# Optimization experiments

Measured on AMD Instinct MI355X. Metric: run time of the kernel, lower is better.

Reference implementation:

```python
import jax, jax.numpy as jnp
import numpy as np

N = 8192
F_IN = 256
F_OUT = 64
ALPHA = 0.2  # LeakyReLU negative slope
MASK_VAL = -9e15


def setup_inputs() -> dict:
    key = jax.random.key(0)
    k1, k2, k3, k4 = jax.random.split(key, 4)
    h = jax.random.normal(k1, (N, F_IN), dtype=jnp.float32)
    adj = jax.random.randint(k2, (N, N), 0, 2, dtype=jnp.int32)  # 0/1 dense adjacency
    # Parameters (original creates them inside forward with xavier init; here fixed inputs)
    W = jax.random.normal(k3, (F_IN, F_OUT), dtype=jnp.float32) * (1.414 * np.sqrt(2.0 / (F_IN + F_OUT)))
    a = jax.random.normal(k4, (2 * F_OUT, 1), dtype=jnp.float32) * (1.414 * np.sqrt(2.0 / (2 * F_OUT + 1)))
    return {"h": h, "adj": adj, "W": W, "a": a}


def reference(h, adj, W, a):
    # Wh: [N, F_OUT]
    Wh = h @ W
    # e_ij = LeakyReLU(a^T [Wh_i ; Wh_j]) computed via broadcast instead of the
    f_src = Wh @ a[:F_OUT, 0]   # [N] contribution of row node i
    f_dst = Wh @ a[F_OUT:, 0]   # [N] contribution of col node j
    e = jax.nn.leaky_relu(f_src[:, None] + f_dst[None, :], negative_slope=ALPHA)  # [N, N]
    # adj-masked row softmax
    scores = jnp.where(adj > 0, e, MASK_VAL)
    attention = jax.nn.softmax(scores, axis=1)
    # dropout omitted (deterministic eval reference)
    h_prime = attention @ Wh  # [N, F_OUT]
    return jax.nn.elu(h_prime)  # concat=True branch
```

## Files before the change

kernel.cpp:

```cpp
#include <hip/hip_runtime.h>
#include <hip/hip_bf16.h>

#define NN 8192
#define FIN 256
#define FOUT 64
#define L2E 1.4426950408889634f
#define PADK3 136

typedef __attribute__((ext_vector_type(8))) short short8;
typedef __attribute__((ext_vector_type(4))) float f32x4;
typedef __attribute__((ext_vector_type(4))) int   iv4;

#define BAR() do { \
  __asm__ __volatile__("s_waitcnt lgkmcnt(0)" ::: "memory"); \
  __builtin_amdgcn_s_barrier(); \
  __asm__ __volatile__("" ::: "memory"); \
} while (0)

__device__ __forceinline__ unsigned short f2bf(float x){
  unsigned u = __float_as_uint(x);
  u += 0x7FFFu + ((u >> 16) & 1u);
  return (unsigned short)(u >> 16);
}

__device__ __forceinline__ unsigned spread4(unsigned x){
  x &= 0xFFu;
  x = (x | (x << 12)) & 0x000F000Fu;
  x = (x | (x << 6))  & 0x03030303u;
  x = (x | (x << 3))  & 0x11111111u;
  return x;
}

__device__ __forceinline__ void cv_process(iv4 d, int l,
                                           unsigned* __restrict__ mp, int g){
  unsigned n = (unsigned)(d.x != 0)        | ((unsigned)(d.y != 0) << 1)
             | ((unsigned)(d.z != 0) << 2) | ((unsigned)(d.w != 0) << 3);
  unsigned long long B0 = __ballot((n & 1u) != 0);
  unsigned long long B1 = __ballot((n & 2u) != 0);
  unsigned long long B2 = __ballot((n & 4u) != 0);
  unsigned long long B3 = __ballot((n & 8u) != 0);
  const int hi = l & 4, sh = (l & 3) * 8;
  unsigned b0 = (unsigned)((hi ? (B0 >> 32) : B0) >> sh);
  unsigned b1 = (unsigned)((hi ? (B1 >> 32) : B1) >> sh);
  unsigned b2 = (unsigned)((hi ? (B2 >> 32) : B2) >> sh);
  unsigned b3 = (unsigned)((hi ? (B3 >> 32) : B3) >> sh);
  unsigned word = spread4(b0) | (spread4(b1) << 1)
                | (spread4(b2) << 2) | (spread4(b3) << 3);
  if (l < 8) mp[g*8 + l] = word;
}

__global__ __launch_bounds__(256) void k_pm(const float* __restrict__ h,
    const float* __restrict__ W, const float* __restrict__ a,
    const int* __restrict__ adj, unsigned short* __restrict__ WhT,
    float* __restrict__ fs, float* __restrict__ fd,
    unsigned* __restrict__ gmax_u, unsigned* __restrict__ mask){
  const int bid = blockIdx.x, t = threadIdx.x;
  const int l = t & 63, wv = t >> 6;
  if (bid % 3 == 0){
    const int pid = bid / 3;
    __shared__ float Ws[128*64];
    __shared__ float hs[8][128];
    const int rb = pid * 8;
    float acc0 = 0.f, acc1 = 0.f;
    for (int half = 0; half < 2; ++half){
      if (half) __syncthreads();
      for (int i = t; i < 2048; i += 256)
        ((float4*)Ws)[i] = ((const float4*)W)[half*2048 + i];
      {
        int rr = t >> 5, cc = t & 31;
        ((float4*)&hs[rr][0])[cc] =
            *(const float4*)(h + (size_t)(rb+rr)*FIN + half*128 + cc*4);
      }
      __syncthreads();
      #pragma unroll 8
      for (int k = 0; k < 128; ++k){
        float wval = Ws[k*64 + l];
        acc0 = fmaf(hs[wv*2+0][k], wval, acc0);
        acc1 = fmaf(hs[wv*2+1][k], wval, acc1);
      }
    }
    const int r0 = rb + wv*2, r1 = r0 + 1;
    float a1 = a[l], a2 = a[64 + l];
    float p0 = acc0*a1, q0 = acc0*a2, p1 = acc1*a1, q1 = acc1*a2;
    #pragma unroll
    for (int m = 1; m < 64; m <<= 1){
      p0 += __shfl_xor(p0, m); q0 += __shfl_xor(q0, m);
      p1 += __shfl_xor(p1, m); q1 += __shfl_xor(q1, m);
    }
    if (l == 0){
      fs[r0] = p0*L2E; fs[r1] = p1*L2E; fd[r0] = q0*L2E; fd[r1] = q1*L2E;
      atomicMax(gmax_u, __float_as_uint(q0*L2E + 64.0f));
      atomicMax(gmax_u, __float_as_uint(q1*L2E + 64.0f));
    }
    WhT[(size_t)l*NN + r0] = f2bf(acc0);
    WhT[(size_t)l*NN + r1] = f2bf(acc1);
  } else {
    const int cid = bid - bid/3 - 1;
    const unsigned rowid = (unsigned)cid*4u + (unsigned)wv;
    const iv4* __restrict__ ap = (const iv4*)(adj + (size_t)rowid*8192u) + l;
    unsigned* __restrict__ mp = mask + rowid*256u;
    iv4 d0 = ap[0*64], d1 = ap[1*64], d2 = ap[2*64], d3 = ap[3*64];
    iv4 d4 = ap[4*64], d5 = ap[5*64], d6 = ap[6*64], d7 = ap[7*64];
    #pragma unroll 1
    for (int i = 0; i < 32; i += 8){
      cv_process(d0, l, mp, i+0); if (i+ 8 < 32) d0 = ap[(i+ 8)*64];
      cv_process(d1, l, mp, i+1); if (i+ 9 < 32) d1 = ap[(i+ 9)*64];
      cv_process(d2, l, mp, i+2); if (i+10 < 32) d2 = ap[(i+10)*64];
      cv_process(d3, l, mp, i+3); if (i+11 < 32) d3 = ap[(i+11)*64];
      cv_process(d4, l, mp, i+4); if (i+12 < 32) d4 = ap[(i+12)*64];
      cv_process(d5, l, mp, i+5); if (i+13 < 32) d5 = ap[(i+13)*64];
      cv_process(d6, l, mp, i+6); if (i+14 < 32) d6 = ap[(i+14)*64];
      cv_process(d7, l, mp, i+7); if (i+15 < 32) d7 = ap[(i+15)*64];
    }
  }
}

__device__ __forceinline__ void attn_math(unsigned mbits, f32x4 fv0, f32x4 fv1,
    short8 w0, short8 w1, short8 w2, short8 w3,
    float fsrL, float mL, f32x4* acc, float& s0, float& s1){
  const float fv[8] = {fv0[0],fv0[1],fv0[2],fv0[3], fv1[0],fv1[1],fv1[2],fv1[3]};
  float w[8];
  #pragma unroll
  for (int j = 0; j < 8; ++j){
    float x  = fsrL + fv[j];
    float tt = fmaxf(x, 0.2f*x);
    float e  = __builtin_amdgcn_exp2f(tt - mL);
    w[j] = (mbits & (1u << j)) ? e : 0.0f;
  }
  s0 += (w[0]+w[2]) + (w[4]+w[6]);
  s1 += (w[1]+w[3]) + (w[5]+w[7]);
  short8 af;
  __hip_bfloat162* afp = (__hip_bfloat162*)&af;
  #pragma unroll
  for (int j = 0; j < 4; ++j)
    afp[j] = __float22bfloat162_rn(make_float2(w[2*j], w[2*j+1]));
  acc[0] = __builtin_amdgcn_mfma_f32_16x16x32_bf16(af, w0, acc[0], 0,0,0);
  acc[1] = __builtin_amdgcn_mfma_f32_16x16x32_bf16(af, w1, acc[1], 0,0,0);
  acc[2] = __builtin_amdgcn_mfma_f32_16x16x32_bf16(af, w2, acc[2], 0,0,0);
  acc[3] = __builtin_amdgcn_mfma_f32_16x16x32_bf16(af, w3, acc[3], 0,0,0);
}

__device__ __forceinline__ void attn_sub(const unsigned short* __restrict__ bs,
    const float* __restrict__ fsl, int sub, int row, int qsh, unsigned mword,
    float fsrL, float mL, f32x4* acc, float& s0, float& s1){
  const int o = sub*32 + qsh;
  f32x4 fv0 = *(const f32x4*)&fsl[o];
  f32x4 fv1 = *(const f32x4*)&fsl[o + 4];
  short8 w0 = *(const short8*)&bs[( 0 + row)*PADK3 + o];
  short8 w1 = *(const short8*)&bs[(16 + row)*PADK3 + o];
  short8 w2 = *(const short8*)&bs[(32 + row)*PADK3 + o];
  short8 w3 = *(const short8*)&bs[(48 + row)*PADK3 + o];
  attn_math(mword >> qsh, fv0, fv1, w0, w1, w2, w3, fsrL, mL, acc, s0, s1);
}

__global__ __launch_bounds__(256, 4) void k_attn(const unsigned* __restrict__ mask,
    const unsigned short* __restrict__ WhT, const float* __restrict__ fs,
    const float* __restrict__ fd, const unsigned* __restrict__ gmax_u,
    float* __restrict__ acc_out, float* __restrict__ s_out){
  __shared__ unsigned short bslab[2][64*PADK3];
  __shared__ float fslab[2][128];
  const int t = threadIdx.x, l = t & 63, wv = t >> 6;
  const int g = blockIdx.x & 127;
  const int kchunk = blockIdx.x >> 7;
  const int row = l & 15, quad = l >> 4;
  const int ibase = g*64 + wv*16;
  const int irow  = ibase + row;
  const float gmaxL = __uint_as_float(*gmax_u) - 64.0f;
  const float fsrL  = fs[irow];
  const float xL    = fsrL + gmaxL;
  const float mL    = fmaxf(xL, 0.2f*xL);

  const unsigned jbase = (unsigned)kchunk*1024u;
  const uint4* __restrict__ mq =
      (const uint4*)(mask + (size_t)irow*256u + (jbase >> 5));
  const unsigned sg_off = (unsigned)l*8192u + jbase + (unsigned)wv*32u;
  const int      sl_off = l*PADK3 + wv*32;
  const int      qsh    = quad*8;

  f32x4 acc[4];
  #pragma unroll
  for (int nb = 0; nb < 4; ++nb) acc[nb] = (f32x4){0.f,0.f,0.f,0.f};

  {
    const unsigned short* p = WhT + sg_off;
    *(short8*)&bslab[0][sl_off]      = *(const short8*)(p);
    *(short8*)&bslab[0][sl_off + 8]  = *(const short8*)(p + 8);
    *(short8*)&bslab[0][sl_off + 16] = *(const short8*)(p + 16);
    *(short8*)&bslab[0][sl_off + 24] = *(const short8*)(p + 24);
    if (t < 128) fslab[0][t] = fd[jbase + t];
  }
  uint4 M0 = mq[0];
  uint4 M1 = mq[1];

  float s0 = 0.f, s1 = 0.f;
  short8 nw0, nw1, nw2, nw3; float nf = 0.f;

  #pragma unroll 1
  for (int s = 0; s < 8; s += 2){
    BAR();
    {
      const unsigned short* p = WhT + sg_off + (s+1)*128;
      nw0 = *(const short8*)(p);
      nw1 = *(const short8*)(p + 8);
      nw2 = *(const short8*)(p + 16);
      nw3 = *(const short8*)(p + 24);
    }
    if (t < 128) nf = fd[jbase + (s+1)*128 + t];
    attn_sub(bslab[0], fslab[0], 0, row, qsh, M0.x, fsrL, mL, acc, s0, s1);
    attn_sub(bslab[0], fslab[0], 1, row, qsh, M0.y, fsrL, mL, acc, s0, s1);
    attn_sub(bslab[0], fslab[0], 2, row, qsh, M0.z, fsrL, mL, acc, s0, s1);
    attn_sub(bslab[0], fslab[0], 3, row, qsh, M0.w, fsrL, mL, acc, s0, s1);
    if (s + 2 < 8) M0 = mq[s + 2];
    *(short8*)&bslab[1][sl_off]      = nw0;
    *(short8*)&bslab[1][sl_off + 8]  = nw1;
    *(short8*)&bslab[1][sl_off + 16] = nw2;
    *(short8*)&bslab[1][sl_off + 24] = nw3;
    if (t < 128) fslab[1][t] = nf;

    BAR();
    if (s + 2 < 8){
      const unsigned short* p = WhT + sg_off + (s+2)*128;
      nw0 = *(const short8*)(p);
      nw1 = *(const short8*)(p + 8);
      nw2 = *(const short8*)(p + 16);
      nw3 = *(const short8*)(p + 24);
      nf = (t < 128) ? fd[jbase + (s+2)*128 + t] : 0.f;
    }
    attn_sub(bslab[1], fslab[1], 0, row, qsh, M1.x, fsrL, mL, acc, s0, s1);
    attn_sub(bslab[1], fslab[1], 1, row, qsh, M1.y, fsrL, mL, acc, s0, s1);
    attn_sub(bslab[1], fslab[1], 2, row, qsh, M1.z, fsrL, mL, acc, s0, s1);
    attn_sub(bslab[1], fslab[1], 3, row, qsh, M1.w, fsrL, mL, acc, s0, s1);
    if (s + 3 < 8) M1 = mq[s + 3];
    if (s + 2 < 8){
      *(short8*)&bslab[0][sl_off]      = nw0;
      *(short8*)&bslab[0][sl_off + 8]  = nw1;
      *(short8*)&bslab[0][sl_off + 16] = nw2;
      *(short8*)&bslab[0][sl_off + 24] = nw3;
      if (t < 128) fslab[0][t] = nf;
    }
  }

  float sacc = s0 + s1;
  sacc += __shfl_xor(sacc, 16);
  sacc += __shfl_xor(sacc, 32);
  if (l < 16) s_out[kchunk*NN + ibase + l] = sacc;
  float* op = acc_out + ((size_t)kchunk*NN + ibase)*FOUT;
  #pragma unroll
  for (int nb = 0; nb < 4; ++nb)
    #pragma unroll
    for (int r = 0; r < 4; ++r)
      op[(quad*4 + r)*FOUT + nb*16 + row] = acc[nb][r];
}

__global__ __launch_bounds__(256) void k_out(const float* __restrict__ acc,
    const float* __restrict__ s, float* __restrict__ out){
  const int idx4 = blockIdx.x*256 + threadIdx.x;
  const int i = idx4 >> 4;
  float4 num = make_float4(0.f,0.f,0.f,0.f);
  float den = 0.f;
  #pragma unroll
  for (int ks = 0; ks < 8; ++ks){
    float4 v = ((const float4*)acc)[idx4 + ks*(NN*FOUT/4)];
    num.x += v.x; num.y += v.y; num.z += v.z; num.w += v.w;
    den += s[i + ks*NN];
  }
  const float rd = 1.0f / den;
  float4 o;
  float x;
  x = num.x*rd; o.x = (x > 0.f) ? x : (__expf(x) - 1.0f);
  x = num.y*rd; o.y = (x > 0.f) ? x : (__expf(x) - 1.0f);
  x = num.z*rd; o.z = (x > 0.f) ? x : (__expf(x) - 1.0f);
  x = num.w*rd; o.w = (x > 0.f) ? x : (__expf(x) - 1.0f);
  ((float4*)out)[idx4] = o;
}

extern "C" void kernel_launch(void* const* d_in, const int* in_sizes, int n_in,
                              void* d_out, int out_size, void* d_ws, size_t ws_size,
                              hipStream_t stream){
  const float* h   = (const float*)d_in[0];
  const int*   adj = (const int*)d_in[1];
  const float* W   = (const float*)d_in[2];
  const float* a   = (const float*)d_in[3];
  char* ws = (char*)d_ws;
  unsigned short* WhT = (unsigned short*)ws;
  float*    fs     = (float*)(ws + (1u<<20));
  float*    fd     = (float*)(ws + (1u<<20) + 32768);
  unsigned* gmax_u = (unsigned*)(ws + (1u<<20) + 65536);
  float*    acc    = (float*)(ws + (2u<<20));
  float*    s_ws   = (float*)(ws + (20u<<20));
  unsigned* mask   = (unsigned*)(ws + (48u<<20));

  (void)hipMemsetAsync(gmax_u, 0, 4, stream);
  k_pm<<<3072, 256, 0, stream>>>(h, W, a, adj, WhT, fs, fd, gmax_u, mask);
  k_attn<<<1024, 256, 0, stream>>>(mask, WhT, fs, fd, gmax_u, acc, s_ws);
  k_out<<<512, 256, 0, stream>>>(acc, s_ws, (float*)d_out);
}
```

Baseline: 504.0 us.

## Double attention block row tile to 128 rows with 512 threads sharing Wh slab

The attention kernel now runs 8 waves per block covering 128 query rows instead of 4 waves covering 64. The staged WhT/fd slab for each key chunk is shared by twice as many rows, so each thread loads half as much (two short8 instead of four). This cuts redundant global-to-LDS traffic per row and halves the grid to 512 blocks, at the cost of fewer blocks and barriers that now synchronise more waves.

```diff
diff --git a/kernel.cpp b/kernel.cpp
--- a/kernel.cpp
+++ b/kernel.cpp
@@ -153,17 +153,17 @@
   attn_math(mword >> qsh, fv0, fv1, w0, w1, w2, w3, fsrL, mL, acc, s0, s1);
 }
 
-__global__ __launch_bounds__(256, 4) void k_attn(const unsigned* __restrict__ mask,
+__global__ __launch_bounds__(512, 4) void k_attn(const unsigned* __restrict__ mask,
     const unsigned short* __restrict__ WhT, const float* __restrict__ fs,
     const float* __restrict__ fd, const unsigned* __restrict__ gmax_u,
     float* __restrict__ acc_out, float* __restrict__ s_out){
   __shared__ unsigned short bslab[2][64*PADK3];
   __shared__ float fslab[2][128];
   const int t = threadIdx.x, l = t & 63, wv = t >> 6;
-  const int g = blockIdx.x & 127;
-  const int kchunk = blockIdx.x >> 7;
+  const int g = blockIdx.x & 63;
+  const int kchunk = blockIdx.x >> 6;
   const int row = l & 15, quad = l >> 4;
-  const int ibase = g*64 + wv*16;
+  const int ibase = g*128 + wv*16;
   const int irow  = ibase + row;
   const float gmaxL = __uint_as_float(*gmax_u) - 64.0f;
   const float fsrL  = fs[irow];
@@ -173,8 +173,8 @@
   const unsigned jbase = (unsigned)kchunk*1024u;
   const uint4* __restrict__ mq =
       (const uint4*)(mask + (size_t)irow*256u + (jbase >> 5));
-  const unsigned sg_off = (unsigned)l*8192u + jbase + (unsigned)wv*32u;
-  const int      sl_off = l*PADK3 + wv*32;
+  const unsigned sg_off = (unsigned)(t & 63)*8192u + jbase + (unsigned)wv*16u;
+  const int      sl_off = (t & 63)*PADK3 + wv*16;
   const int      qsh    = quad*8;
 
   f32x4 acc[4];
@@ -182,48 +182,35 @@
   for (int nb = 0; nb < 4; ++nb) acc[nb] = (f32x4){0.f,0.f,0.f,0.f};
 
   {
-    const unsigned short* p = WhT + sg_off;
-    *(short8*)&bslab[0][sl_off]      = *(const short8*)(p);
-    *(short8*)&bslab[0][sl_off + 8]  = *(const short8*)(p + 8);
-    *(short8*)&bslab[0][sl_off + 16] = *(const short8*)(p + 16);
-    *(short8*)&bslab[0][sl_off + 24] = *(const short8*)(p + 24);
+    *(short8*)&bslab[0][sl_off]     = *(const short8*)(WhT + sg_off);
+    *(short8*)&bslab[0][sl_off + 8] = *(const short8*)(WhT + sg_off + 8);
     if (t < 128) fslab[0][t] = fd[jbase + t];
   }
   uint4 M0 = mq[0];
   uint4 M1 = mq[1];
 
   float s0 = 0.f, s1 = 0.f;
-  short8 nw0, nw1, nw2, nw3; float nf = 0.f;
+  short8 nwa, nwb; float nf = 0.f;
 
   #pragma unroll 1
   for (int s = 0; s < 8; s += 2){
     BAR();
-    {
-      const unsigned short* p = WhT + sg_off + (s+1)*128;
-      nw0 = *(const short8*)(p);
-      nw1 = *(const short8*)(p + 8);
-      nw2 = *(const short8*)(p + 16);
-      nw3 = *(const short8*)(p + 24);
-    }
+    nwa = *(const short8*)(WhT + sg_off + (s+1)*128);
+    nwb = *(const short8*)(WhT + sg_off + (s+1)*128 + 8);
     if (t < 128) nf = fd[jbase + (s+1)*128 + t];
     attn_sub(bslab[0], fslab[0], 0, row, qsh, M0.x, fsrL, mL, acc, s0, s1);
     attn_sub(bslab[0], fslab[0], 1, row, qsh, M0.y, fsrL, mL, acc, s0, s1);
     attn_sub(bslab[0], fslab[0], 2, row, qsh, M0.z, fsrL, mL, acc, s0, s1);
     attn_sub(bslab[0], fslab[0], 3, row, qsh, M0.w, fsrL, mL, acc, s0, s1);
     if (s + 2 < 8) M0 = mq[s + 2];
-    *(short8*)&bslab[1][sl_off]      = nw0;
-    *(short8*)&bslab[1][sl_off + 8]  = nw1;
-    *(short8*)&bslab[1][sl_off + 16] = nw2;
-    *(short8*)&bslab[1][sl_off + 24] = nw3;
+    *(short8*)&bslab[1][sl_off]     = nwa;
+    *(short8*)&bslab[1][sl_off + 8] = nwb;
     if (t < 128) fslab[1][t] = nf;
 
     BAR();
     if (s + 2 < 8){
-      const unsigned short* p = WhT + sg_off + (s+2)*128;
-      nw0 = *(const short8*)(p);
-      nw1 = *(const short8*)(p + 8);
-      nw2 = *(const short8*)(p + 16);
-      nw3 = *(const short8*)(p + 24);
+      nwa = *(const short8*)(WhT + sg_off + (s+2)*128);
+      nwb = *(const short8*)(WhT + sg_off + (s+2)*128 + 8);
       nf = (t < 128) ? fd[jbase + (s+2)*128 + t] : 0.f;
     }
     attn_sub(bslab[1], fslab[1], 0, row, qsh, M1.x, fsrL, mL, acc, s0, s1);
@@ -232,10 +219,8 @@
     attn_sub(bslab[1], fslab[1], 3, row, qsh, M1.w, fsrL, mL, acc, s0, s1);
     if (s + 3 < 8) M1 = mq[s + 3];
     if (s + 2 < 8){
-      *(short8*)&bslab[0][sl_off]      = nw0;
-      *(short8*)&bslab[0][sl_off + 8]  = nw1;
-      *(short8*)&bslab[0][sl_off + 16] = nw2;
-      *(short8*)&bslab[0][sl_off + 24] = nw3;
+      *(short8*)&bslab[0][sl_off]     = nwa;
+      *(short8*)&bslab[0][sl_off + 8] = nwb;
       if (t < 128) fslab[0][t] = nf;
     }
   }
@@ -292,6 +277,6 @@
 
   (void)hipMemsetAsync(gmax_u, 0, 4, stream);
   k_pm<<<3072, 256, 0, stream>>>(h, W, a, adj, WhT, fs, fd, gmax_u, mask);
-  k_attn<<<1024, 256, 0, stream>>>(mask, WhT, fs, fd, gmax_u, acc, s_ws);
+  k_attn<<<512, 512, 0, stream>>>(mask, WhT, fs, fd, gmax_u, acc, s_ws);
   k_out<<<512, 256, 0, stream>>>(acc, s_ws, (float*)d_out);
 }
```

New measurement: 481.7 us. 4.4% less time.
